# Performance work log

Hardware: AMD Instinct MI355X
Metric: run time of the kernel (lower is better)

## Reference

```python
import jax, jax.numpy as jnp
import numpy as np

N = 20000
D = 64


def gcn_conv(x, src, dst, ew, W, b, n_nodes):
    # PyG GCNConv: lin -> gcn_norm (with self loops) -> scatter-add -> +bias
    loop = jnp.arange(n_nodes)
    s = jnp.concatenate([src, loop])
    d = jnp.concatenate([dst, loop])
    w = jnp.concatenate([ew, jnp.ones((n_nodes,), ew.dtype)])
    deg = jax.ops.segment_sum(w, d, num_segments=n_nodes)
    dinv = jnp.where(deg > 0, jax.lax.rsqrt(deg), 0.0)
    norm = dinv[s] * w * dinv[d]  # [E+N]
    h = x @ W  # [N, D]
    msg = h[s] * norm[:, None]  # gather + scale
    out = jax.ops.segment_sum(msg, d, num_segments=n_nodes)  # scatter-add
    return out + b


def layernorm(x, gamma, beta, eps=1e-5):
    mu = jnp.mean(x, axis=-1, keepdims=True)
    var = jnp.var(x, axis=-1, keepdims=True)
    return (x - mu) * jax.lax.rsqrt(var + eps) * gamma + beta


def setup_inputs() -> dict:
    key = jax.random.key(0)
    ks = jax.random.split(key, 12)
    E = 640000
    x = jax.random.normal(ks[0], (N, D), jnp.float32)
    edge_index = jax.random.randint(ks[1], (2, E), 0, N, jnp.int64)
    edge_weight = jax.random.uniform(ks[2], (E,), jnp.float32)
    glorot = 1.0 / np.sqrt(D)
    Wc1 = jax.random.uniform(ks[3], (D, D), jnp.float32, -glorot, glorot)
    bc1 = jnp.zeros((D,), jnp.float32)
    Wc2 = jax.random.uniform(ks[4], (D, D), jnp.float32, -glorot, glorot)
    bc2 = jnp.zeros((D,), jnp.float32)
    # xavier_uniform on (num_labels*D, D) view: bound = sqrt(6/(D+D))
    bnd = np.sqrt(6.0 / (2 * D))
    W1 = jax.random.uniform(ks[5], (N, D, D), jnp.float32, -bnd, bnd)
    b1 = jnp.zeros((N, D), jnp.float32)
    W2 = jax.random.uniform(ks[6], (N, D, D), jnp.float32, -bnd, bnd)
    b2 = jnp.zeros((N, D), jnp.float32)
    ln_gamma = jnp.ones((D,), jnp.float32)
    ln_beta = jnp.zeros((D,), jnp.float32)
    return {"x": x, "edge_index": edge_index, "edge_weight": edge_weight,
            "Wc1": Wc1, "bc1": bc1, "Wc2": Wc2, "bc2": bc2,
            "W1": W1, "b1": b1, "W2": W2, "b2": b2,
            "ln_gamma": ln_gamma, "ln_beta": ln_beta}


def reference(x, edge_index, edge_weight, Wc1, bc1, Wc2, bc2, W1, b1, W2, b2, ln_gamma, ln_beta):
    src, dst = edge_index[0], edge_index[1]
    h = gcn_conv(x, src, dst, edge_weight, Wc1, bc1, N)
    h = jax.nn.selu(h)
    h = gcn_conv(h, src, dst, edge_weight, Wc2, bc2, N)
    h = jax.nn.selu(h)
    # per-node label-specific transform (num_labels == N)
    t = jnp.einsum('nd,ndj->nj', h, W1) + b1
    t = layernorm(t, ln_gamma, ln_beta)
    t = jnp.einsum('nd,ndj->nj', t, W2) + b2
    return t
```

## Files before the change

### kernel.cpp

```cpp
#include <hip/hip_runtime.h>
#include <stdint.h>

#define ND 64

typedef __attribute__((ext_vector_type(4))) float floatx4;
typedef __attribute__((ext_vector_type(4))) short shortx4;
typedef __attribute__((ext_vector_type(8))) short short8;
typedef unsigned long long u64;

__device__ __forceinline__ float bf2f(unsigned short u) {
  union { unsigned int i; float f; } v; v.i = ((unsigned int)u) << 16; return v.f;
}
__device__ __forceinline__ unsigned short f2bf(float f) {
  union { float f; unsigned int i; } v; v.f = f;
  unsigned int x = v.i;
  return (unsigned short)((x + 0x7fffu + ((x >> 16) & 1u)) >> 16);
}
__device__ __forceinline__ float selu_f(float x) {
  float r = x > 0.f ? x : 1.6732632423543772f * expm1f(x);
  return 1.0507009873554805f * r;
}
__device__ __forceinline__ bool is_bf16_data(const void* gam) {
  return ((const unsigned short*)gam)[0] == 0x3F80;
}
__device__ __forceinline__ float ldE(const void* p, size_t i, bool bf) {
  return bf ? bf2f(((const unsigned short*)p)[i]) : ((const float*)p)[i];
}
__device__ __forceinline__ floatx4 ld4(const void* p, size_t i, bool bf) {
  floatx4 r;
  if (bf) {
    shortx4 v = *(const shortx4*)((const unsigned short*)p + i);
#pragma unroll
    for (int k = 0; k < 4; ++k) r[k] = bf2f((unsigned short)v[k]);
  } else {
    r = *(const floatx4*)((const float*)p + i);
  }
  return r;
}

__global__ void k_pre(u64* packed, int n) {
  int i = blockIdx.x * blockDim.x + threadIdx.x;
  if (i < n) packed[i] = 16777216ULL;
}

__global__ void k_deg(const int* __restrict__ dst, const void* __restrict__ ew,
                      u64* packed, int E, const void* __restrict__ gam) {
  bool bf = is_bf16_data(gam);
  int e = blockIdx.x * blockDim.x + threadIdx.x;
  if (e < E) {
    float w = ldE(ew, e, bf);
    u64 a = (1ULL << 48) | (u64)(long long)(w * 16777216.0f + 0.5f);
    atomicAdd(&packed[dst[e]], a);
  }
}

__global__ __launch_bounds__(1024) void k_scan(const u64* __restrict__ packed,
                                               float* __restrict__ dinv,
                                               int* __restrict__ row_ptr,
                                               int* __restrict__ cursor, int n) {
  extern __shared__ int lds[];
  __shared__ int part[1024];
  int t = threadIdx.x;
  for (int i = t; i < n; i += 1024) {
    u64 p = packed[i];
    lds[i] = (int)(p >> 48);
    float g = (float)(p & 0xFFFFFFFFFFFFULL) * 5.9604644775390625e-8f;
    dinv[i] = g > 0.f ? rsqrtf(g) : 0.f;
  }
  __syncthreads();
  int C = (n + 1023) >> 10;
  int base = t * C;
  int lim = base + C; if (lim > n) lim = n;
  int s = 0;
  for (int i = base; i < lim; ++i) s += lds[i];
  part[t] = s;
  __syncthreads();
  for (int off = 1; off < 1024; off <<= 1) {
    int v = (t >= off) ? part[t - off] : 0;
    __syncthreads();
    if (t >= off) part[t] += v;
    __syncthreads();
  }
  int run = (t == 0) ? 0 : part[t - 1];
  for (int i = base; i < lim; ++i) { int c = lds[i]; lds[i] = run; run += c; }
  __syncthreads();
  for (int i = t; i < n; i += 1024) { int v = lds[i]; row_ptr[i] = v; cursor[i] = v; }
  if (t == 0) row_ptr[n] = part[1023];
}

__global__ void k_fill(const int* __restrict__ src, const int* __restrict__ dst,
                       const void* __restrict__ ew, const float* __restrict__ dinv,
                       int* cursor, u64* __restrict__ csr, int E,
                       const void* __restrict__ gam) {
  bool bf = is_bf16_data(gam);
  int e = blockIdx.x * blockDim.x + threadIdx.x;
  if (e < E) {
    int s = src[e], d = dst[e];
    float nm = dinv[s] * ldE(ew, e, bf) * dinv[d];
    int pos = atomicAdd(&cursor[d], 1);
    csr[pos] = ((u64)__float_as_uint(nm) << 32) | (unsigned int)s;
  }
}

template <int IN_EXT>
__global__ __launch_bounds__(256) void k_gemm(const void* __restrict__ X,
                                              const void* __restrict__ Wc,
                                              unsigned short* __restrict__ H, int n,
                                              const void* __restrict__ gam) {
  bool bf = is_bf16_data(gam);
  int lane = threadIdx.x & 63;
  int jg = lane & 15, dg = lane >> 4;
  float w[16][4];
#pragma unroll
  for (int dd = 0; dd < 16; ++dd) {
    floatx4 v = ld4(Wc, (size_t)(dd * 4 + dg) * 64 + jg * 4, bf);
#pragma unroll
    for (int k = 0; k < 4; ++k) w[dd][k] = v[k];
  }
  int wave = (blockIdx.x * blockDim.x + threadIdx.x) >> 6;
  int nw = (gridDim.x * blockDim.x) >> 6;
  for (int nn = wave; nn < n; nn += nw) {
    float hreg = IN_EXT ? ldE(X, (size_t)nn * 64 + lane, bf)
                        : ((const float*)X)[(size_t)nn * 64 + lane];
    float acc[4] = {0.f, 0.f, 0.f, 0.f};
#pragma unroll
    for (int dd = 0; dd < 16; ++dd) {
      float hv = __shfl(hreg, dd * 4 + dg);
#pragma unroll
      for (int k = 0; k < 4; ++k) acc[k] += hv * w[dd][k];
    }
#pragma unroll
    for (int k = 0; k < 4; ++k) acc[k] += __shfl_xor(acc[k], 16);
#pragma unroll
    for (int k = 0; k < 4; ++k) acc[k] += __shfl_xor(acc[k], 32);
    if (lane < 16) {
      shortx4 o;
#pragma unroll
      for (int k = 0; k < 4; ++k) o[k] = (short)f2bf(acc[k]);
      *(shortx4*)(H + (size_t)nn * 64 + lane * 4) = o;
    }
  }
}

__global__ __launch_bounds__(256) void k_agg(const unsigned short* __restrict__ h,
                                             const int* __restrict__ row_ptr,
                                             const u64* __restrict__ csr,
                                             const float* __restrict__ dinv,
                                             const void* __restrict__ bias,
                                             float* __restrict__ outp, int n,
                                             const void* __restrict__ gam) {
  bool bf = is_bf16_data(gam);
  int wv = (blockIdx.x * blockDim.x + threadIdx.x) >> 6;
  int lane = threadIdx.x & 63;
  if (wv >= n) return;
  float di = dinv[wv];
  float a0 = di * di * bf2f(h[(size_t)wv * 64 + lane]);
  float a1 = 0.f, a2 = 0.f, a3 = 0.f;
  int k = row_ptr[wv], end = row_ptr[wv + 1];
  while (k < end) {
    int cnt = end - k;
    if (cnt > 64) cnt = 64;
    u64 mv = 0;
    if (lane < cnt) mv = csr[k + lane];
    int j = 0;
    for (; j + 4 <= cnt; j += 4) {
      u64 v0 = __shfl(mv, j), v1 = __shfl(mv, j + 1);
      u64 v2 = __shfl(mv, j + 2), v3 = __shfl(mv, j + 3);
      float h0 = bf2f(h[(size_t)(unsigned int)(v0 & 0xFFFFFFFFu) * 64 + lane]);
      float h1 = bf2f(h[(size_t)(unsigned int)(v1 & 0xFFFFFFFFu) * 64 + lane]);
      float h2 = bf2f(h[(size_t)(unsigned int)(v2 & 0xFFFFFFFFu) * 64 + lane]);
      float h3 = bf2f(h[(size_t)(unsigned int)(v3 & 0xFFFFFFFFu) * 64 + lane]);
      a0 += __uint_as_float((unsigned int)(v0 >> 32)) * h0;
      a1 += __uint_as_float((unsigned int)(v1 >> 32)) * h1;
      a2 += __uint_as_float((unsigned int)(v2 >> 32)) * h2;
      a3 += __uint_as_float((unsigned int)(v3 >> 32)) * h3;
    }
    for (; j < cnt; ++j) {
      u64 v = __shfl(mv, j);
      a0 += __uint_as_float((unsigned int)(v >> 32)) *
            bf2f(h[(size_t)(unsigned int)(v & 0xFFFFFFFFu) * 64 + lane]);
    }
    k += cnt;
  }
  float acc = (a0 + a1) + (a2 + a3) + ldE(bias, lane, bf);
  outp[(size_t)wv * 64 + lane] = selu_f(acc);
}

__global__ __launch_bounds__(256) void k_fused(const float* __restrict__ g2,
                                               const void* __restrict__ W1,
                                               const void* __restrict__ b1,
                                               const void* __restrict__ W2,
                                               const void* __restrict__ b2,
                                               const void* __restrict__ gam,
                                               const void* __restrict__ bet,
                                               void* __restrict__ out, int n) {
  __shared__ float tbuf[4][64];
  bool bf = is_bf16_data(gam);
  int wid = threadIdx.x >> 6;
  int lane = threadIdx.x & 63;
  int nn = blockIdx.x * 4 + wid;
  if (nn >= n) nn = n - 1;
  float hreg = g2[(size_t)nn * 64 + lane];
  size_t Wb = (size_t)nn * 4096;

  if (bf) {
    int jg = lane & 7, dg = lane >> 3;
    int j0 = jg * 8;
    const unsigned short* W1p = (const unsigned short*)W1 + Wb;
    const unsigned short* W2p = (const unsigned short*)W2 + Wb;
    float acc[8];
#pragma unroll
    for (int k = 0; k < 8; ++k) acc[k] = 0.f;
#pragma unroll
    for (int dd = 0; dd < 8; ++dd) {
      int d = dd * 8 + dg;
      float hv = __shfl(hreg, d);
      short8 w = *(const short8*)(W1p + d * 64 + j0);
#pragma unroll
      for (int k = 0; k < 8; ++k) acc[k] += hv * bf2f((unsigned short)w[k]);
    }
#pragma unroll
    for (int m = 8; m <= 32; m <<= 1)
#pragma unroll
      for (int k = 0; k < 8; ++k) acc[k] += __shfl_xor(acc[k], m);
    short8 bb = *(const short8*)((const unsigned short*)b1 + (size_t)nn * 64 + j0);
#pragma unroll
    for (int k = 0; k < 8; ++k) acc[k] += bf2f((unsigned short)bb[k]);

    float s1 = 0.f, s2 = 0.f;
#pragma unroll
    for (int k = 0; k < 8; ++k) { s1 += acc[k]; s2 += acc[k] * acc[k]; }
#pragma unroll
    for (int m = 1; m <= 4; m <<= 1) { s1 += __shfl_xor(s1, m); s2 += __shfl_xor(s2, m); }
    float mean = s1 * (1.f / 64.f);
    float var = s2 * (1.f / 64.f) - mean * mean;
    if (var < 0.f) var = 0.f;
    float rinv = rsqrtf(var + 1e-5f);
    short8 gm = *(const short8*)((const unsigned short*)gam + j0);
    short8 bt = *(const short8*)((const unsigned short*)bet + j0);
    float tn[8];
#pragma unroll
    for (int k = 0; k < 8; ++k)
      tn[k] = (acc[k] - mean) * rinv * bf2f((unsigned short)gm[k]) + bf2f((unsigned short)bt[k]);
    if (lane < 8) {
#pragma unroll
      for (int k = 0; k < 8; ++k) tbuf[wid][lane * 8 + k] = tn[k];
    }
    __syncthreads();

    float acc2[8];
#pragma unroll
    for (int k = 0; k < 8; ++k) acc2[k] = 0.f;
#pragma unroll
    for (int dd = 0; dd < 8; ++dd) {
      int d = dd * 8 + dg;
      float tv = tbuf[wid][d];
      short8 w = *(const short8*)(W2p + d * 64 + j0);
#pragma unroll
      for (int k = 0; k < 8; ++k) acc2[k] += tv * bf2f((unsigned short)w[k]);
    }
#pragma unroll
    for (int m = 8; m <= 32; m <<= 1)
#pragma unroll
      for (int k = 0; k < 8; ++k) acc2[k] += __shfl_xor(acc2[k], m);
    short8 b2v = *(const short8*)((const unsigned short*)b2 + (size_t)nn * 64 + j0);
#pragma unroll
    for (int k = 0; k < 8; ++k) acc2[k] += bf2f((unsigned short)b2v[k]);
    if (lane < 8) {
      short8 o;
#pragma unroll
      for (int k = 0; k < 8; ++k) o[k] = (short)f2bf(acc2[k]);
      *(short8*)((unsigned short*)out + (size_t)nn * 64 + lane * 8) = o;
    }
  } else {
    int jg = lane & 15, dg = lane >> 4;
    int j0 = jg * 4;
    const float* W1p = (const float*)W1 + Wb;
    const float* W2p = (const float*)W2 + Wb;
    float acc[4] = {0.f, 0.f, 0.f, 0.f};
#pragma unroll
    for (int dd = 0; dd < 16; ++dd) {
      int d = dd * 4 + dg;
      float hv = __shfl(hreg, d);
      floatx4 w = *(const floatx4*)(W1p + d * 64 + j0);
#pragma unroll
      for (int k = 0; k < 4; ++k) acc[k] += hv * w[k];
    }
#pragma unroll
    for (int m = 16; m <= 32; m <<= 1)
#pragma unroll
      for (int k = 0; k < 4; ++k) acc[k] += __shfl_xor(acc[k], m);
    floatx4 bb = *(const floatx4*)((const float*)b1 + (size_t)nn * 64 + j0);
#pragma unroll
    for (int k = 0; k < 4; ++k) acc[k] += bb[k];

    float s1 = 0.f, s2 = 0.f;
#pragma unroll
    for (int k = 0; k < 4; ++k) { s1 += acc[k]; s2 += acc[k] * acc[k]; }
#pragma unroll
    for (int m = 1; m <= 8; m <<= 1) { s1 += __shfl_xor(s1, m); s2 += __shfl_xor(s2, m); }
    float mean = s1 * (1.f / 64.f);
    float var = s2 * (1.f / 64.f) - mean * mean;
    if (var < 0.f) var = 0.f;
    float rinv = rsqrtf(var + 1e-5f);
    floatx4 gm = *(const floatx4*)((const float*)gam + j0);
    floatx4 bt = *(const floatx4*)((const float*)bet + j0);
    float tn[4];
#pragma unroll
    for (int k = 0; k < 4; ++k) tn[k] = (acc[k] - mean) * rinv * gm[k] + bt[k];
    if (lane < 16) {
#pragma unroll
      for (int k = 0; k < 4; ++k) tbuf[wid][lane * 4 + k] = tn[k];
    }
    __syncthreads();

    float acc2[4] = {0.f, 0.f, 0.f, 0.f};
#pragma unroll
    for (int dd = 0; dd < 16; ++dd) {
      int d = dd * 4 + dg;
      float tv = tbuf[wid][d];
      floatx4 w = *(const floatx4*)(W2p + d * 64 + j0);
#pragma unroll
      for (int k = 0; k < 4; ++k) acc2[k] += tv * w[k];
    }
#pragma unroll
    for (int m = 16; m <= 32; m <<= 1)
#pragma unroll
      for (int k = 0; k < 4; ++k) acc2[k] += __shfl_xor(acc2[k], m);
    floatx4 b2v = *(const floatx4*)((const float*)b2 + (size_t)nn * 64 + j0);
#pragma unroll
    for (int k = 0; k < 4; ++k) acc2[k] += b2v[k];
    if (lane < 16) {
      floatx4 o = {acc2[0], acc2[1], acc2[2], acc2[3]};
      *(floatx4*)((float*)out + (size_t)nn * 64 + lane * 4) = o;
    }
  }
}

extern "C" void kernel_launch(void* const* d_in, const int* in_sizes, int n_in,
                              void* d_out, int out_size, void* d_ws, size_t ws_size,
                              hipStream_t stream) {
  const int N = in_sizes[0] / ND;
  const int E = in_sizes[2];
  const void* x   = d_in[0];
  const int* ei   = (const int*)d_in[1];
  const void* ew  = d_in[2];
  const void* Wc1 = d_in[3];
  const void* bc1 = d_in[4];
  const void* Wc2 = d_in[5];
  const void* bc2 = d_in[6];
  const void* W1  = d_in[7];
  const void* b1  = d_in[8];
  const void* W2  = d_in[9];
  const void* b2  = d_in[10];
  const void* gam = d_in[11];
  const void* bet = d_in[12];
  const int* srcp = ei;
  const int* dstp = ei + E;

  char* ws = (char*)d_ws;
  size_t off = 0;
  auto take = [&](size_t bytes) {
    void* p = ws + off;
    off = (off + bytes + 255) & ~(size_t)255;
    return p;
  };
  u64* packed     = (u64*)take((size_t)N * 8);
  float* dinv     = (float*)take((size_t)N * 4);
  int* row_ptr    = (int*)take((size_t)(N + 1) * 4);
  int* cursor     = (int*)take((size_t)N * 4);
  u64* csr        = (u64*)take((size_t)E * 8);
  unsigned short* h = (unsigned short*)take((size_t)N * ND * 2);
  float* g1       = (float*)take((size_t)N * ND * 4);
  float* g2       = (float*)take((size_t)N * ND * 4);
  (void)ws_size; (void)n_in; (void)out_size;

  k_pre<<<(N + 255) / 256, 256, 0, stream>>>(packed, N);
  k_deg<<<(E + 255) / 256, 256, 0, stream>>>(dstp, ew, packed, E, gam);
  k_scan<<<1, 1024, (size_t)N * 4, stream>>>(packed, dinv, row_ptr, cursor, N);
  k_fill<<<(E + 255) / 256, 256, 0, stream>>>(srcp, dstp, ew, dinv, cursor, csr, E, gam);
  k_gemm<1><<<256, 256, 0, stream>>>(x, Wc1, h, N, gam);
  k_agg<<<(N + 3) / 4, 256, 0, stream>>>(h, row_ptr, csr, dinv, bc1, g1, N, gam);
  k_gemm<0><<<256, 256, 0, stream>>>(g1, Wc2, h, N, gam);
  k_agg<<<(N + 3) / 4, 256, 0, stream>>>(h, row_ptr, csr, dinv, bc2, g2, N, gam);
  k_fused<<<(N + 3) / 4, 256, 0, stream>>>(g2, W1, b1, W2, b2, gam, bet, d_out, N);
}
```

Baseline: 785.5 us.

## Fuse second GCN layer with per-node transforms using aggregate-then-transform reordering

The second GCN layer is reordered to aggregate the bf16 layer-1 output first and then multiply by Wc2, which is staged in shared memory. This lets the aggregation, linear, SELU, per-node W1/LayerNorm/W2 stages run in one kernel. Layer-1 output is now stored as bf16 instead of fp32, and the shared-memory handoff plus __syncthreads in the LayerNorm stage is replaced with lane shuffles. The goal is to remove two kernel launches and the intermediate global round-trips, at the cost of a 16KB Wc2 load per block and bf16 rounding of an intermediate.

```diff
diff --git a/kernel.cpp b/kernel.cpp
--- a/kernel.cpp
+++ b/kernel.cpp
@@ -147,7 +147,7 @@
                                              const u64* __restrict__ csr,
                                              const float* __restrict__ dinv,
                                              const void* __restrict__ bias,
-                                             float* __restrict__ outp, int n,
+                                             unsigned short* __restrict__ outp, int n,
                                              const void* __restrict__ gam) {
   bool bf = is_bf16_data(gam);
   int wv = (blockIdx.x * blockDim.x + threadIdx.x) >> 6;
@@ -183,26 +183,91 @@
     k += cnt;
   }
   float acc = (a0 + a1) + (a2 + a3) + ldE(bias, lane, bf);
-  outp[(size_t)wv * 64 + lane] = selu_f(acc);
-}
-
-__global__ __launch_bounds__(256) void k_fused(const float* __restrict__ g2,
-                                               const void* __restrict__ W1,
-                                               const void* __restrict__ b1,
-                                               const void* __restrict__ W2,
-                                               const void* __restrict__ b2,
-                                               const void* __restrict__ gam,
-                                               const void* __restrict__ bet,
-                                               void* __restrict__ out, int n) {
-  __shared__ float tbuf[4][64];
+  outp[(size_t)wv * 64 + lane] = f2bf(selu_f(acc));
+}
+
+__global__ __launch_bounds__(256) void k_l2fused(const unsigned short* __restrict__ g1,
+                                                 const int* __restrict__ row_ptr,
+                                                 const u64* __restrict__ csr,
+                                                 const float* __restrict__ dinv,
+                                                 const void* __restrict__ Wc2,
+                                                 const void* __restrict__ bc2,
+                                                 const void* __restrict__ W1,
+                                                 const void* __restrict__ b1,
+                                                 const void* __restrict__ W2,
+                                                 const void* __restrict__ b2,
+                                                 const void* __restrict__ gam,
+                                                 const void* __restrict__ bet,
+                                                 void* __restrict__ out, int n) {
+  __shared__ float wcs[4096];
   bool bf = is_bf16_data(gam);
-  int wid = threadIdx.x >> 6;
-  int lane = threadIdx.x & 63;
+  int tid = threadIdx.x;
+  for (int i = tid * 4; i < 4096; i += 1024) {
+    floatx4 v = ld4(Wc2, i, bf);
+    *(floatx4*)&wcs[i] = v;
+  }
+  __syncthreads();
+
+  int wid = tid >> 6, lane = tid & 63;
   int nn = blockIdx.x * 4 + wid;
   if (nn >= n) nn = n - 1;
-  float hreg = g2[(size_t)nn * 64 + lane];
+
+  float di = dinv[nn];
+  float a0 = di * di * bf2f(g1[(size_t)nn * 64 + lane]);
+  float a1 = 0.f, a2 = 0.f, a3 = 0.f;
+  int k = row_ptr[nn], end = row_ptr[nn + 1];
+  while (k < end) {
+    int cnt = end - k;
+    if (cnt > 64) cnt = 64;
+    u64 mv = 0;
+    if (lane < cnt) mv = csr[k + lane];
+    int j = 0;
+    for (; j + 4 <= cnt; j += 4) {
+      u64 v0 = __shfl(mv, j), v1 = __shfl(mv, j + 1);
+      u64 v2 = __shfl(mv, j + 2), v3 = __shfl(mv, j + 3);
+      float h0 = bf2f(g1[(size_t)(unsigned int)(v0 & 0xFFFFFFFFu) * 64 + lane]);
+      float h1 = bf2f(g1[(size_t)(unsigned int)(v1 & 0xFFFFFFFFu) * 64 + lane]);
+      float h2 = bf2f(g1[(size_t)(unsigned int)(v2 & 0xFFFFFFFFu) * 64 + lane]);
+      float h3 = bf2f(g1[(size_t)(unsigned int)(v3 & 0xFFFFFFFFu) * 64 + lane]);
+      a0 += __uint_as_float((unsigned int)(v0 >> 32)) * h0;
+      a1 += __uint_as_float((unsigned int)(v1 >> 32)) * h1;
+      a2 += __uint_as_float((unsigned int)(v2 >> 32)) * h2;
+      a3 += __uint_as_float((unsigned int)(v3 >> 32)) * h3;
+    }
+    for (; j < cnt; ++j) {
+      u64 v = __shfl(mv, j);
+      a0 += __uint_as_float((unsigned int)(v >> 32)) *
+            bf2f(g1[(size_t)(unsigned int)(v & 0xFFFFFFFFu) * 64 + lane]);
+    }
+    k += cnt;
+  }
+  float agg = (a0 + a1) + (a2 + a3);
+
+  int jm = lane & 15, dm = lane >> 4;
+  float acm[4] = {0.f, 0.f, 0.f, 0.f};
+#pragma unroll
+  for (int dd = 0; dd < 16; ++dd) {
+    int d = dd * 4 + dm;
+    float hv = __shfl(agg, d);
+    floatx4 w = *(const floatx4*)&wcs[d * 64 + jm * 4];
+#pragma unroll
+    for (int q = 0; q < 4; ++q) acm[q] += hv * w[q];
+  }
+#pragma unroll
+  for (int q = 0; q < 4; ++q) acm[q] += __shfl_xor(acm[q], 16);
+#pragma unroll
+  for (int q = 0; q < 4; ++q) acm[q] += __shfl_xor(acm[q], 32);
+  floatx4 bb2 = ld4(bc2, jm * 4, bf);
+#pragma unroll
+  for (int q = 0; q < 4; ++q) acm[q] = selu_f(acm[q] + bb2[q]);
+  float c0 = __shfl(acm[0], lane >> 2);
+  float c1 = __shfl(acm[1], lane >> 2);
+  float c2 = __shfl(acm[2], lane >> 2);
+  float c3 = __shfl(acm[3], lane >> 2);
+  int r2 = lane & 3;
+  float hreg = r2 == 0 ? c0 : r2 == 1 ? c1 : r2 == 2 ? c2 : c3;
+
   size_t Wb = (size_t)nn * 4096;
-
   if (bf) {
     int jg = lane & 7, dg = lane >> 3;
     int j0 = jg * 8;
@@ -210,26 +275,26 @@
     const unsigned short* W2p = (const unsigned short*)W2 + Wb;
     float acc[8];
 #pragma unroll
-    for (int k = 0; k < 8; ++k) acc[k] = 0.f;
+    for (int q = 0; q < 8; ++q) acc[q] = 0.f;
 #pragma unroll
     for (int dd = 0; dd < 8; ++dd) {
       int d = dd * 8 + dg;
       float hv = __shfl(hreg, d);
       short8 w = *(const short8*)(W1p + d * 64 + j0);
 #pragma unroll
-      for (int k = 0; k < 8; ++k) acc[k] += hv * bf2f((unsigned short)w[k]);
+      for (int q = 0; q < 8; ++q) acc[q] += hv * bf2f((unsigned short)w[q]);
     }
 #pragma unroll
     for (int m = 8; m <= 32; m <<= 1)
 #pragma unroll
-      for (int k = 0; k < 8; ++k) acc[k] += __shfl_xor(acc[k], m);
+      for (int q = 0; q < 8; ++q) acc[q] += __shfl_xor(acc[q], m);
     short8 bb = *(const short8*)((const unsigned short*)b1 + (size_t)nn * 64 + j0);
 #pragma unroll
-    for (int k = 0; k < 8; ++k) acc[k] += bf2f((unsigned short)bb[k]);
+    for (int q = 0; q < 8; ++q) acc[q] += bf2f((unsigned short)bb[q]);
 
     float s1 = 0.f, s2 = 0.f;
 #pragma unroll
-    for (int k = 0; k < 8; ++k) { s1 += acc[k]; s2 += acc[k] * acc[k]; }
+    for (int q = 0; q < 8; ++q) { s1 += acc[q]; s2 += acc[q] * acc[q]; }
 #pragma unroll
     for (int m = 1; m <= 4; m <<= 1) { s1 += __shfl_xor(s1, m); s2 += __shfl_xor(s2, m); }
     float mean = s1 * (1.f / 64.f);
@@ -240,36 +305,42 @@
     short8 bt = *(const short8*)((const unsigned short*)bet + j0);
     float tn[8];
 #pragma unroll
-    for (int k = 0; k < 8; ++k)
-      tn[k] = (acc[k] - mean) * rinv * bf2f((unsigned short)gm[k]) + bf2f((unsigned short)bt[k]);
-    if (lane < 8) {
-#pragma unroll
-      for (int k = 0; k < 8; ++k) tbuf[wid][lane * 8 + k] = tn[k];
-    }
-    __syncthreads();
+    for (int q = 0; q < 8; ++q)
+      tn[q] = (acc[q] - mean) * rinv * bf2f((unsigned short)gm[q]) + bf2f((unsigned short)bt[q]);
+    float e0 = __shfl(tn[0], lane >> 3);
+    float e1 = __shfl(tn[1], lane >> 3);
+    float e2 = __shfl(tn[2], lane >> 3);
+    float e3 = __shfl(tn[3], lane >> 3);
+    float e4 = __shfl(tn[4], lane >> 3);
+    float e5 = __shfl(tn[5], lane >> 3);
+    float e6 = __shfl(tn[6], lane >> 3);
+    float e7 = __shfl(tn[7], lane >> 3);
+    int r8 = lane & 7;
+    float tfull = r8 == 0 ? e0 : r8 == 1 ? e1 : r8 == 2 ? e2 : r8 == 3 ? e3
+                : r8 == 4 ? e4 : r8 == 5 ? e5 : r8 == 6 ? e6 : e7;
 
     float acc2[8];
 #pragma unroll
-    for (int k = 0; k < 8; ++k) acc2[k] = 0.f;
+    for (int q = 0; q < 8; ++q) acc2[q] = 0.f;
 #pragma unroll
     for (int dd = 0; dd < 8; ++dd) {
       int d = dd * 8 + dg;
-      float tv = tbuf[wid][d];
+      float tv = __shfl(tfull, d);
       short8 w = *(const short8*)(W2p + d * 64 + j0);
 #pragma unroll
-      for (int k = 0; k < 8; ++k) acc2[k] += tv * bf2f((unsigned short)w[k]);
+      for (int q = 0; q < 8; ++q) acc2[q] += tv * bf2f((unsigned short)w[q]);
     }
 #pragma unroll
     for (int m = 8; m <= 32; m <<= 1)
 #pragma unroll
-      for (int k = 0; k < 8; ++k) acc2[k] += __shfl_xor(acc2[k], m);
+      for (int q = 0; q < 8; ++q) acc2[q] += __shfl_xor(acc2[q], m);
     short8 b2v = *(const short8*)((const unsigned short*)b2 + (size_t)nn * 64 + j0);
 #pragma unroll
-    for (int k = 0; k < 8; ++k) acc2[k] += bf2f((unsigned short)b2v[k]);
+    for (int q = 0; q < 8; ++q) acc2[q] += bf2f((unsigned short)b2v[q]);
     if (lane < 8) {
       short8 o;
 #pragma unroll
-      for (int k = 0; k < 8; ++k) o[k] = (short)f2bf(acc2[k]);
+      for (int q = 0; q < 8; ++q) o[q] = (short)f2bf(acc2[q]);
       *(short8*)((unsigned short*)out + (size_t)nn * 64 + lane * 8) = o;
     }
   } else {
@@ -284,19 +355,19 @@
       float hv = __shfl(hreg, d);
       floatx4 w = *(const floatx4*)(W1p + d * 64 + j0);
 #pragma unroll
-      for (int k = 0; k < 4; ++k) acc[k] += hv * w[k];
+      for (int q = 0; q < 4; ++q) acc[q] += hv * w[q];
     }
 #pragma unroll
     for (int m = 16; m <= 32; m <<= 1)
 #pragma unroll
-      for (int k = 0; k < 4; ++k) acc[k] += __shfl_xor(acc[k], m);
+      for (int q = 0; q < 4; ++q) acc[q] += __shfl_xor(acc[q], m);
     floatx4 bb = *(const floatx4*)((const float*)b1 + (size_t)nn * 64 + j0);
 #pragma unroll
-    for (int k = 0; k < 4; ++k) acc[k] += bb[k];
+    for (int q = 0; q < 4; ++q) acc[q] += bb[q];
 
     float s1 = 0.f, s2 = 0.f;
 #pragma unroll
-    for (int k = 0; k < 4; ++k) { s1 += acc[k]; s2 += acc[k] * acc[k]; }
+    for (int q = 0; q < 4; ++q) { s1 += acc[q]; s2 += acc[q] * acc[q]; }
 #pragma unroll
     for (int m = 1; m <= 8; m <<= 1) { s1 += __shfl_xor(s1, m); s2 += __shfl_xor(s2, m); }
     float mean = s1 * (1.f / 64.f);
@@ -307,29 +378,30 @@
     floatx4 bt = *(const floatx4*)((const float*)bet + j0);
     float tn[4];
 #pragma unroll
-    for (int k = 0; k < 4; ++k) tn[k] = (acc[k] - mean) * rinv * gm[k] + bt[k];
-    if (lane < 16) {
-#pragma unroll
-      for (int k = 0; k < 4; ++k) tbuf[wid][lane * 4 + k] = tn[k];
-    }
-    __syncthreads();
+    for (int q = 0; q < 4; ++q) tn[q] = (acc[q] - mean) * rinv * gm[q] + bt[q];
+    float e0 = __shfl(tn[0], lane >> 2);
+    float e1 = __shfl(tn[1], lane >> 2);
+    float e2 = __shfl(tn[2], lane >> 2);
+    float e3 = __shfl(tn[3], lane >> 2);
+    int r4 = lane & 3;
+    float tfull = r4 == 0 ? e0 : r4 == 1 ? e1 : r4 == 2 ? e2 : e3;
 
     float acc2[4] = {0.f, 0.f, 0.f, 0.f};
 #pragma unroll
     for (int dd = 0; dd < 16; ++dd) {
       int d = dd * 4 + dg;
-      float tv = tbuf[wid][d];
+      float tv = __shfl(tfull, d);
       floatx4 w = *(const floatx4*)(W2p + d * 64 + j0);
 #pragma unroll
-      for (int k = 0; k < 4; ++k) acc2[k] += tv * w[k];
+      for (int q = 0; q < 4; ++q) acc2[q] += tv * w[q];
     }
 #pragma unroll
     for (int m = 16; m <= 32; m <<= 1)
 #pragma unroll
-      for (int k = 0; k < 4; ++k) acc2[k] += __shfl_xor(acc2[k], m);
+      for (int q = 0; q < 4; ++q) acc2[q] += __shfl_xor(acc2[q], m);
     floatx4 b2v = *(const floatx4*)((const float*)b2 + (size_t)nn * 64 + j0);
 #pragma unroll
-    for (int k = 0; k < 4; ++k) acc2[k] += b2v[k];
+    for (int q = 0; q < 4; ++q) acc2[q] += b2v[q];
     if (lane < 16) {
       floatx4 o = {acc2[0], acc2[1], acc2[2], acc2[3]};
       *(floatx4*)((float*)out + (size_t)nn * 64 + lane * 4) = o;
@@ -370,9 +442,8 @@
   int* row_ptr    = (int*)take((size_t)(N + 1) * 4);
   int* cursor     = (int*)take((size_t)N * 4);
   u64* csr        = (u64*)take((size_t)E * 8);
-  unsigned short* h = (unsigned short*)take((size_t)N * ND * 2);
-  float* g1       = (float*)take((size_t)N * ND * 4);
-  float* g2       = (float*)take((size_t)N * ND * 4);
+  unsigned short* h  = (unsigned short*)take((size_t)N * ND * 2);
+  unsigned short* g1 = (unsigned short*)take((size_t)N * ND * 2);
   (void)ws_size; (void)n_in; (void)out_size;
 
   k_pre<<<(N + 255) / 256, 256, 0, stream>>>(packed, N);
@@ -381,7 +452,6 @@
   k_fill<<<(E + 255) / 256, 256, 0, stream>>>(srcp, dstp, ew, dinv, cursor, csr, E, gam);
   k_gemm<1><<<256, 256, 0, stream>>>(x, Wc1, h, N, gam);
   k_agg<<<(N + 3) / 4, 256, 0, stream>>>(h, row_ptr, csr, dinv, bc1, g1, N, gam);
-  k_gemm<0><<<256, 256, 0, stream>>>(g1, Wc2, h, N, gam);
-  k_agg<<<(N + 3) / 4, 256, 0, stream>>>(h, row_ptr, csr, dinv, bc2, g2, N, gam);
-  k_fused<<<(N + 3) / 4, 256, 0, stream>>>(g2, W1, b1, W2, b2, gam, bet, d_out, N);
-}
+  k_l2fused<<<(N + 3) / 4, 256, 0, stream>>>(g1, row_ptr, csr, dinv, Wc2, bc2,
+                                             W1, b1, W2, b2, gam, bet, d_out, N);
+}
```

Result: no change. 772.1 us (-1.7%).
